# Performance work log

Hardware: AMD Instinct MI355X
Metric: run time of the kernel (lower is better)

## Reference

```python
import jax, jax.numpy as jnp
import numpy as np

N_PTS = 65536      # query points (ray samples)
N_NODES = 4096     # deformation-graph nodes
K = 20             # neighbors, hardcoded in the module
D_PE = 32          # positional-encoding channels (sliced off, unused)
DIS_THRESH = 0.00021
FAR_VAL = 1e9


def setup_inputs() -> dict:
    key = jax.random.key(0)
    k1, k2, k3, k4, k5 = jax.random.split(key, 5)
    inputs = jax.random.normal(k1, (N_PTS, 3 + D_PE), dtype=jnp.float32)
    vd = jax.random.normal(k2, (N_NODES, 3), dtype=jnp.float32)
    R = jax.random.normal(k3, (N_NODES, 3, 3), dtype=jnp.float32)
    g = jax.random.normal(k4, (N_NODES, 3), dtype=jnp.float32)
    t = jax.random.normal(k5, (N_NODES, 3), dtype=jnp.float32) * 0.1
    return {"inputs": inputs, "vd": vd, "R": R, "g": g, "t": t}


def reference(inputs, vd, R, g, t):
    pts = inputs[:, :3]  # [N,3]; inputs[:,3:] (positional encoding) is unused

    # --- KNN (knn_points semantics: squared L2 dists, ascending) ---
    d2 = (jnp.sum(pts * pts, axis=-1, keepdims=True)
          + jnp.sum(vd * vd, axis=-1)[None, :]
          - 2.0 * pts @ vd.T)                      # [N, n]
    neg_d, idx = jax.lax.top_k(-d2, K)             # smallest d2 first
    dis = -neg_d                                   # [N,K] squared dists, ascending

    # --- neighbor weights: w = (1 - d/d_max)^2, normalized ---
    dis_max = jnp.max(dis, axis=-1, keepdims=True)
    w = jnp.square(1.0 - dis / dis_max)
    w = w / jnp.sum(w, axis=-1, keepdims=True)     # [N,K] (K=20 > 1, so no ones override)

    # --- per-neighbor gather + rigid transform: p = R^T (x - g - t) + g ---
    Rg = R[idx]                                    # [N,K,3,3]
    gg = g[idx]                                    # [N,K,3]
    tg = t[idx]                                    # [N,K,3]
    x = pts[:, None, :] - gg - tg                  # [N,K,3]
    p = jnp.einsum('nkji,nkj->nki', Rg, x) + gg    # R^T @ x, [N,K,3]
    R_inv = jnp.swapaxes(Rg, -1, -2)               # [N,K,3,3]

    # --- weighted blend over K neighbors ---
    p_blend = jnp.sum(p * w[:, :, None], axis=1)               # [N,3]
    R_blend = jnp.sum(R_inv * w[:, :, None, None], axis=1)     # [N,3,3]

    # --- far-point masking on x-coordinate ---
    far = dis[:, 0] > DIS_THRESH
    p_blend = p_blend.at[:, 0].set(jnp.where(far, FAR_VAL, p_blend[:, 0]))
    return p_blend, R_blend
```

## Files before the change

kernel.cpp:

```cpp
#include <hip/hip_runtime.h>
#include <stdint.h>


#define NPTS   65536
#define NNODES 4096
#define KSEL   20
#define CAP    32
#define BT     256
#define AFRAG_BYTES  (NNODES * 64)
#define WS_NEEDED    (AFRAG_BYTES + NNODES * 4)

typedef __attribute__((ext_vector_type(8)))  short short8;
typedef __attribute__((ext_vector_type(16))) float f32x16;

__device__ __forceinline__ uint32_t umin32(uint32_t a, uint32_t b) { return a < b ? a : b; }
__device__ __forceinline__ uint32_t umax32(uint32_t a, uint32_t b) { return a > b ? a : b; }
__device__ __forceinline__ void cmpswap(uint32_t& a, uint32_t& b) {
  const uint32_t lo = umin32(a, b), hi = umax32(a, b); a = lo; b = hi;
}
__device__ __forceinline__ void insert20(uint32_t m[KSEL], uint32_t x) {
#pragma unroll
  for (int k = KSEL - 1; k >= 1; --k)
    m[k] = umin32(m[k], umax32(m[k - 1], x));
  m[0] = umin32(m[0], x);
}
__device__ __forceinline__ float thr_from(uint32_t m19) {
  return __uint_as_float(umin32((m19 >> 12) << 11, 0x7F7FFFFFu));
}
__device__ __forceinline__ unsigned short f2bf(float x) {
  uint32_t u = __float_as_uint(x);
  return (unsigned short)((u + 0x7FFFu + ((u >> 16) & 1u)) >> 16);
}
__device__ __forceinline__ float bf2f(unsigned short h) {
  return __uint_as_float(((uint32_t)h) << 16);
}

__global__ void dg_prep(const float* __restrict__ vd,
                        unsigned short* __restrict__ aF, float* __restrict__ svP) {
  const int j = blockIdx.x * 256 + threadIdx.x;
  const float v0 = vd[j * 3 + 0], v1 = vd[j * 3 + 1], v2 = vd[j * 3 + 2];
  unsigned short H[3], M[3], L[3];
  const float vc[3] = {v0, v1, v2};
#pragma unroll
  for (int c = 0; c < 3; ++c) {
    H[c] = f2bf(vc[c]);
    const float r1 = vc[c] - bf2f(H[c]);
    M[c] = f2bf(r1);
    const float r2 = r1 - bf2f(M[c]);
    L[c] = f2bf(r2);
  }
  unsigned short* o = aF + j * 32;
  o[0]=H[0]; o[1]=H[1]; o[2]=H[2]; o[3]=M[0]; o[4]=M[1]; o[5]=M[2];
  o[6]=L[0]; o[7]=L[1]; o[8]=L[2]; o[9]=H[0]; o[10]=H[1]; o[11]=H[2];
  o[12]=M[0]; o[13]=M[1]; o[14]=M[2]; o[15]=L[0];
  o[16]=L[1]; o[17]=L[2]; o[18]=H[0]; o[19]=H[1]; o[20]=H[2];
  o[21]=M[0]; o[22]=M[1]; o[23]=M[2]; o[24]=L[0]; o[25]=L[1]; o[26]=L[2];
  o[27]=0; o[28]=0; o[29]=0; o[30]=0; o[31]=0;
  const int row = j & 31, t = j >> 5;
  const int h = (row >> 2) & 1;
  const int i = (row & 3) + 4 * (row >> 3);
  svP[t * 32 + h * 16 + i] = v0 * v0 + v1 * v1 + v2 * v2;
}

__global__ __launch_bounds__(BT, 4) void dg_mfma(
    const float* __restrict__ inp, const float* __restrict__ vd,
    const float* __restrict__ Rm, const float* __restrict__ gv,
    const float* __restrict__ tv, const short8* __restrict__ aF,
    const float4* __restrict__ svP, float* __restrict__ out)
{
  __shared__ uint32_t st[CAP * BT];
  const int tid  = threadIdx.x;
  const int lane = tid & 63;
  const int col  = lane & 31;
  const int h    = lane >> 5;
  const int wv   = tid >> 6;
  const int half = wv & 1;
  const int pg   = wv >> 1;
  const int P    = pg * 32 + col;
  const int gi   = blockIdx.x * 64 + P;

  const float p0 = inp[gi * 35 + 0];
  const float p1 = inp[gi * 35 + 1];
  const float p2 = inp[gi * 35 + 2];
  const float sp = p0 * p0 + p1 * p1 + p2 * p2;

  unsigned short qH[3], qM[3], qL[3];
  {
    const float qc[3] = {-2.0f * p0, -2.0f * p1, -2.0f * p2};
#pragma unroll
    for (int c = 0; c < 3; ++c) {
      qH[c] = f2bf(qc[c]);
      const float r1 = qc[c] - bf2f(qH[c]);
      qM[c] = f2bf(r1);
      const float r2 = r1 - bf2f(qM[c]);
      qL[c] = f2bf(r2);
    }
  }
  short8 b1, b2;
  if (h == 0) {
    b1[0]=qH[0]; b1[1]=qH[1]; b1[2]=qH[2]; b1[3]=qH[0];
    b1[4]=qH[1]; b1[5]=qH[2]; b1[6]=qH[0]; b1[7]=qH[1];
    b2[0]=qM[1]; b2[1]=qM[2]; b2[2]=qL[0]; b2[3]=qL[1];
    b2[4]=qL[2]; b2[5]=qL[0]; b2[6]=qL[1]; b2[7]=qL[2];
  } else {
    b1[0]=qH[2]; b1[1]=qM[0]; b1[2]=qM[1]; b1[3]=qM[2];
    b1[4]=qM[0]; b1[5]=qM[1]; b1[6]=qM[2]; b1[7]=qM[0];
    b2[0]=qL[0]; b2[1]=qL[1]; b2[2]=qL[2]; b2[3]=0;
    b2[4]=0; b2[5]=0; b2[6]=0; b2[7]=0;
  }

  uint32_t m[KSEL];
#pragma unroll
  for (int k = 0; k < KSEL; ++k) m[k] = 0xFFFFFFFFu;
  uint32_t cnt = 0;
  float thr = __uint_as_float(0x7F7FFFFFu);

  auto drain = [&]() {
    for (uint32_t u = 0; u < cnt; ++u) {
      const uint32_t x = st[u * BT + tid];
      if (x < m[KSEL - 1]) insert20(m, x);
    }
    cnt = 0;
    uint32_t k19 = m[KSEL - 1];
    k19 = umin32(k19, (uint32_t)__shfl_xor((int)k19, 32));
    thr = thr_from(k19);
  };

  const int T0 = half * 64;
  const short8* ap = aF + ((size_t)(T0 * 32 + col) * 64 + (size_t)h * 16) / 16;
  const float4* sv = svP + ((size_t)T0 * 32 + (size_t)h * 16) / 4;
  uint32_t nb = (uint32_t)(T0 * 32 + 4 * h);

#pragma unroll 1
  for (int t = 0; t < 64; ++t) {
    const short8 a1 = ap[0];
    const short8 a2 = ap[2];
    const float4 s0 = sv[0], s1 = sv[1], s2 = sv[2], s3 = sv[3];
    f32x16 acc;
    acc[0]=sp+s0.x;  acc[1]=sp+s0.y;  acc[2]=sp+s0.z;  acc[3]=sp+s0.w;
    acc[4]=sp+s1.x;  acc[5]=sp+s1.y;  acc[6]=sp+s1.z;  acc[7]=sp+s1.w;
    acc[8]=sp+s2.x;  acc[9]=sp+s2.y;  acc[10]=sp+s2.z; acc[11]=sp+s2.w;
    acc[12]=sp+s3.x; acc[13]=sp+s3.y; acc[14]=sp+s3.z; acc[15]=sp+s3.w;
    acc = __builtin_amdgcn_mfma_f32_32x32x16_bf16(a1, b1, acc, 0, 0, 0);
    acc = __builtin_amdgcn_mfma_f32_32x32x16_bf16(a2, b2, acc, 0, 0, 0);
#pragma unroll
    for (int i = 0; i < 16; ++i) {
      const float d = acc[i];
      const uint32_t key =
          ((__float_as_uint(fmaxf(d, 0.0f)) & 0xFFFFF800u) << 1)
          + (nb + (uint32_t)((i & 3) + 8 * (i >> 2)));
      st[cnt * BT + tid] = key;
      cnt += (uint32_t)(d < thr);
    }
    if (__any((int)(cnt >= 16))) drain();
    ap += 4 * 32;
    sv += 8;
    nb += 32;
  }
  drain();

  uint32_t arr[32];
#pragma unroll
  for (int k = 0; k < KSEL; ++k) arr[k] = m[k];
#pragma unroll
  for (int k = KSEL; k < 32; ++k) arr[k] = 0xFFFFFFFFu;
#pragma unroll
  for (int k = 0; k < 16; ++k) {
    const uint32_t sa = (uint32_t)__shfl_xor((int)arr[k],      32);
    const uint32_t sb = (uint32_t)__shfl_xor((int)arr[31 - k], 32);
    arr[k]      = umin32(arr[k],      sb);
    arr[31 - k] = umin32(arr[31 - k], sa);
  }
#pragma unroll
  for (int dd = 16; dd >= 1; dd >>= 1)
#pragma unroll
    for (int k = 0; k < 32; ++k)
      if ((k & dd) == 0) cmpswap(arr[k], arr[k | dd]);

  __syncthreads();
  if (half == 1 && h == 0) {
    uint32_t* mb = st + P * KSEL;
#pragma unroll
    for (int k = 0; k < KSEL; ++k) mb[k] = arr[k];
  }
  __syncthreads();
  if (half == 1) return;

  uint32_t sset[KSEL];
  {
    const uint32_t* mb = st + P * KSEL;
#pragma unroll
    for (int k = 0; k < KSEL; ++k)
      sset[k] = umin32(arr[k], mb[KSEL - 1 - k]);
  }

  int   id10[10];
  float d10[10];
  float dmn = 1e30f, dmx = -1e30f;
#pragma unroll
  for (int s = 0; s < 10; ++s) {
    const int idk = (int)(sset[2 * s + h] & 0xFFFu);
    id10[s] = idk;
    const float v0 = vd[idk * 3 + 0];
    const float v1 = vd[idk * 3 + 1];
    const float v2 = vd[idk * 3 + 2];
    const float sv2 = v0 * v0 + v1 * v1 + v2 * v2;
    const float dt  = p0 * v0 + p1 * v1 + p2 * v2;
    const float ddx = (sp + sv2) - 2.0f * dt;
    d10[s] = ddx;
    dmn = fminf(dmn, ddx);
    dmx = fmaxf(dmx, ddx);
  }
  dmx = fmaxf(dmx, __shfl_xor(dmx, 32));
  dmn = fminf(dmn, __shfl_xor(dmn, 32));

  const float invmax = 1.0f / dmx;
  float wsum = 0.0f, pb0 = 0.0f, pb1 = 0.0f, pb2 = 0.0f;
  float rb[9];
#pragma unroll
  for (int a2i = 0; a2i < 9; ++a2i) rb[a2i] = 0.0f;

#pragma unroll
  for (int s = 0; s < 10; ++s) {
    const int idk = id10[s];
    const float u = 1.0f - d10[s] * invmax;
    const float w = u * u;
    wsum += w;
    const float* Rp = Rm + idk * 9;
    const float r00 = Rp[0], r01 = Rp[1], r02 = Rp[2];
    const float r10 = Rp[3], r11 = Rp[4], r12 = Rp[5];
    const float r20 = Rp[6], r21 = Rp[7], r22 = Rp[8];
    const float g0 = gv[idk * 3 + 0];
    const float g1 = gv[idk * 3 + 1];
    const float g2 = gv[idk * 3 + 2];
    const float t0 = tv[idk * 3 + 0];
    const float t1 = tv[idk * 3 + 1];
    const float t2 = tv[idk * 3 + 2];
    const float x0 = p0 - g0 - t0;
    const float x1 = p1 - g1 - t1;
    const float x2 = p2 - g2 - t2;
    pb0 += w * (r00 * x0 + r10 * x1 + r20 * x2 + g0);
    pb1 += w * (r01 * x0 + r11 * x1 + r21 * x2 + g1);
    pb2 += w * (r02 * x0 + r12 * x1 + r22 * x2 + g2);
    rb[0] += w * r00; rb[1] += w * r10; rb[2] += w * r20;
    rb[3] += w * r01; rb[4] += w * r11; rb[5] += w * r21;
    rb[6] += w * r02; rb[7] += w * r12; rb[8] += w * r22;
  }

  wsum += __shfl_xor(wsum, 32);
  pb0  += __shfl_xor(pb0, 32);
  pb1  += __shfl_xor(pb1, 32);
  pb2  += __shfl_xor(pb2, 32);
#pragma unroll
  for (int a2i = 0; a2i < 9; ++a2i) rb[a2i] += __shfl_xor(rb[a2i], 32);

  if (h == 0) {
    const float inw = 1.0f / wsum;
    float o0 = pb0 * inw;
    if (dmn > 0.00021f) o0 = 1000000000.0f;
    float* po = out + (size_t)gi * 3;
    po[0] = o0; po[1] = pb1 * inw; po[2] = pb2 * inw;
    float* ro = out + (size_t)NPTS * 3 + (size_t)gi * 9;
#pragma unroll
    for (int a2i = 0; a2i < 9; ++a2i) ro[a2i] = rb[a2i] * inw;
  }
}

__global__ __launch_bounds__(BT, 4) void dg_fb(
    const float* __restrict__ inp, const float* __restrict__ vd,
    const float* __restrict__ Rm, const float* __restrict__ gv,
    const float* __restrict__ tv, float* __restrict__ out)
{
  __shared__ uint32_t st[33 * BT];
  const int tid = threadIdx.x;
  const int q   = (tid >> 4) & 3;
  const int pl  = tid & 15;
  const int wv  = tid >> 6;
  const int gi  = blockIdx.x * 64 + wv * 16 + pl;
  const float p0 = inp[gi * 35 + 0];
  const float p1 = inp[gi * 35 + 1];
  const float p2 = inp[gi * 35 + 2];
  const float sp = p0 * p0 + p1 * p1 + p2 * p2;
  uint32_t m[KSEL];
#pragma unroll
  for (int k = 0; k < KSEL; ++k) m[k] = 0xFFFFFFFFu;
  int cnt = 0;
  float thr = __uint_as_float(0x7F7FFFFFu);
  const int jbase = q * (NNODES / 4);
  int lo = 0;
#pragma unroll
  for (int c = 0; c < 6; ++c) {
    const int hi = 32 << c;
    for (int i = lo; i < hi; ++i) {
      const int j = jbase + i;
      const float v0 = vd[j * 3 + 0], v1 = vd[j * 3 + 1], v2 = vd[j * 3 + 2];
      const float sv = v0 * v0 + v1 * v1 + v2 * v2;
      const float dt = p0 * v0 + p1 * v1 + p2 * v2;
      float d2 = fmaxf((sp + sv) - 2.0f * dt, 0.0f);
      if (d2 < thr) {
        st[cnt * BT + tid] = ((__float_as_uint(d2) & 0xFFFFF800u) << 1) | (uint32_t)j;
        if (++cnt == 33) {
          for (int u = 0; u < cnt; ++u) {
            const uint32_t x = st[u * BT + tid];
            if (x < m[KSEL - 1]) insert20(m, x);
          }
          cnt = 0; thr = thr_from(m[KSEL - 1]);
        }
      }
    }
    for (int u = 0; u < cnt; ++u) {
      const uint32_t x = st[u * BT + tid];
      if (x < m[KSEL - 1]) insert20(m, x);
    }
    cnt = 0; thr = thr_from(m[KSEL - 1]); lo = hi;
  }
  uint32_t arr[32];
#pragma unroll
  for (int k = 0; k < KSEL; ++k) arr[k] = m[k];
#pragma unroll
  for (int k = KSEL; k < 32; ++k) arr[k] = 0xFFFFFFFFu;
#pragma unroll
  for (int mask = 32; mask >= 16; mask >>= 1) {
#pragma unroll
    for (int k = 0; k < 16; ++k) {
      const uint32_t sa = (uint32_t)__shfl_xor((int)arr[k],      mask);
      const uint32_t sb = (uint32_t)__shfl_xor((int)arr[31 - k], mask);
      arr[k]      = umin32(arr[k],      sb);
      arr[31 - k] = umin32(arr[31 - k], sa);
    }
#pragma unroll
    for (int dd = 16; dd >= 1; dd >>= 1)
#pragma unroll
      for (int k = 0; k < 32; ++k)
        if ((k & dd) == 0) cmpswap(arr[k], arr[k | dd]);
  }
  int id5[5]; float d5[5];
  float dmn = 1e30f, dmx = -1e30f;
#pragma unroll
  for (int s = 0; s < 5; ++s) {
    const int idk = (int)(arr[4 * s + q] & 0xFFFu);
    id5[s] = idk;
    const float v0 = vd[idk * 3 + 0], v1 = vd[idk * 3 + 1], v2 = vd[idk * 3 + 2];
    const float sv = v0 * v0 + v1 * v1 + v2 * v2;
    const float dt = p0 * v0 + p1 * v1 + p2 * v2;
    const float ddx = (sp + sv) - 2.0f * dt;
    d5[s] = ddx; dmn = fminf(dmn, ddx); dmx = fmaxf(dmx, ddx);
  }
#pragma unroll
  for (int r = 16; r <= 32; r <<= 1) {
    dmx = fmaxf(dmx, __shfl_xor(dmx, r));
    dmn = fminf(dmn, __shfl_xor(dmn, r));
  }
  const float invmax = 1.0f / dmx;
  float wsum = 0.0f, pb0 = 0.0f, pb1 = 0.0f, pb2 = 0.0f;
  float rb[9];
#pragma unroll
  for (int a2i = 0; a2i < 9; ++a2i) rb[a2i] = 0.0f;
#pragma unroll
  for (int s = 0; s < 5; ++s) {
    const int idk = id5[s];
    const float u = 1.0f - d5[s] * invmax;
    const float w = u * u;
    wsum += w;
    const float* Rp = Rm + idk * 9;
    const float r00 = Rp[0], r01 = Rp[1], r02 = Rp[2];
    const float r10 = Rp[3], r11 = Rp[4], r12 = Rp[5];
    const float r20 = Rp[6], r21 = Rp[7], r22 = Rp[8];
    const float g0 = gv[idk * 3 + 0], g1 = gv[idk * 3 + 1], g2 = gv[idk * 3 + 2];
    const float t0 = tv[idk * 3 + 0], t1 = tv[idk * 3 + 1], t2 = tv[idk * 3 + 2];
    const float x0 = p0 - g0 - t0, x1 = p1 - g1 - t1, x2 = p2 - g2 - t2;
    pb0 += w * (r00 * x0 + r10 * x1 + r20 * x2 + g0);
    pb1 += w * (r01 * x0 + r11 * x1 + r21 * x2 + g1);
    pb2 += w * (r02 * x0 + r12 * x1 + r22 * x2 + g2);
    rb[0] += w * r00; rb[1] += w * r10; rb[2] += w * r20;
    rb[3] += w * r01; rb[4] += w * r11; rb[5] += w * r21;
    rb[6] += w * r02; rb[7] += w * r12; rb[8] += w * r22;
  }
#pragma unroll
  for (int r = 16; r <= 32; r <<= 1) {
    wsum += __shfl_xor(wsum, r);
    pb0 += __shfl_xor(pb0, r);
    pb1 += __shfl_xor(pb1, r);
    pb2 += __shfl_xor(pb2, r);
#pragma unroll
    for (int a2i = 0; a2i < 9; ++a2i) rb[a2i] += __shfl_xor(rb[a2i], r);
  }
  if (q == 0) {
    const float inw = 1.0f / wsum;
    float o0 = pb0 * inw;
    if (dmn > 0.00021f) o0 = 1000000000.0f;
    float* po = out + (size_t)gi * 3;
    po[0] = o0; po[1] = pb1 * inw; po[2] = pb2 * inw;
    float* ro = out + (size_t)NPTS * 3 + (size_t)gi * 9;
#pragma unroll
    for (int a2i = 0; a2i < 9; ++a2i) ro[a2i] = rb[a2i] * inw;
  }
}

extern "C" void kernel_launch(void* const* d_in, const int* in_sizes, int n_in,
                              void* d_out, int out_size, void* d_ws, size_t ws_size,
                              hipStream_t stream) {
  const float* inp = (const float*)d_in[0];
  const float* vd  = (const float*)d_in[1];
  const float* Rm  = (const float*)d_in[2];
  const float* gv  = (const float*)d_in[3];
  const float* tv  = (const float*)d_in[4];
  float* out = (float*)d_out;

  if (ws_size >= (size_t)WS_NEEDED) {
    unsigned short* aF = (unsigned short*)d_ws;
    float* svt = (float*)((char*)d_ws + AFRAG_BYTES);
    dg_prep<<<NNODES / 256, 256, 0, stream>>>(vd, aF, svt);
    dg_mfma<<<NPTS / 64, BT, 0, stream>>>(inp, vd, Rm, gv, tv,
                                          (const short8*)aF,
                                          (const float4*)svt, out);
  } else {
    dg_fb<<<NPTS / 64, BT, 0, stream>>>(inp, vd, Rm, gv, tv, out);
  }
}
```

Measured before the change: 163.5 us.

## Split KNN node scan across four waves per point group with tree merge

Each block now handles 32 points instead of 64, and the 4096 nodes are split into four quarters, one per wave, so each wave scans 32 tiles instead of 64. The four partial top-20 lists are combined in a two-level tree merge through shared memory, with a 32-wide bitonic sort at each level. The grid is doubled and the candidate staging buffer shrinks from 32 to 20 slots per thread, which lowers LDS use and may raise occupancy. In exchange, the drain threshold drops to 4 pending candidates, so drains happen more often, and the extra merge stage adds barriers and sorting work.

```diff
diff --git a/kernel.cpp b/kernel.cpp
--- a/kernel.cpp
+++ b/kernel.cpp
@@ -5,7 +5,7 @@
 #define NPTS   65536
 #define NNODES 4096
 #define KSEL   20
-#define CAP    32
+#define CAP    20
 #define BT     256
 #define AFRAG_BYTES  (NNODES * 64)
 #define WS_NEEDED    (AFRAG_BYTES + NNODES * 4)
@@ -33,6 +33,13 @@
 }
 __device__ __forceinline__ float bf2f(unsigned short h) {
   return __uint_as_float(((uint32_t)h) << 16);
+}
+__device__ __forceinline__ void sort32(uint32_t arr[32]) {
+#pragma unroll
+  for (int dd = 16; dd >= 1; dd >>= 1)
+#pragma unroll
+    for (int k = 0; k < 32; ++k)
+      if ((k & dd) == 0) cmpswap(arr[k], arr[k | dd]);
 }
 
 __global__ void dg_prep(const float* __restrict__ vd,
@@ -73,11 +80,8 @@
   const int lane = tid & 63;
   const int col  = lane & 31;
   const int h    = lane >> 5;
-  const int wv   = tid >> 6;
-  const int half = wv & 1;
-  const int pg   = wv >> 1;
-  const int P    = pg * 32 + col;
-  const int gi   = blockIdx.x * 64 + P;
+  const int q    = tid >> 6;
+  const int gi   = blockIdx.x * 32 + col;
 
   const float p0 = inp[gi * 35 + 0];
   const float p1 = inp[gi * 35 + 1];
@@ -126,13 +130,13 @@
     thr = thr_from(k19);
   };
 
-  const int T0 = half * 64;
-  const short8* ap = aF + ((size_t)(T0 * 32 + col) * 64 + (size_t)h * 16) / 16;
-  const float4* sv = svP + ((size_t)T0 * 32 + (size_t)h * 16) / 4;
+  const int T0 = q * 32;
+  const short8* ap = aF + ((T0 * 32 + col) * 4 + h);
+  const float4* sv = svP + (T0 * 8 + h * 4);
   uint32_t nb = (uint32_t)(T0 * 32 + 4 * h);
 
 #pragma unroll 1
-  for (int t = 0; t < 64; ++t) {
+  for (int t = 0; t < 32; ++t) {
     const short8 a1 = ap[0];
     const short8 a2 = ap[2];
     const float4 s0 = sv[0], s1 = sv[1], s2 = sv[2], s3 = sv[3];
@@ -152,8 +156,8 @@
       st[cnt * BT + tid] = key;
       cnt += (uint32_t)(d < thr);
     }
-    if (__any((int)(cnt >= 16))) drain();
-    ap += 4 * 32;
+    if (__any((int)(cnt >= CAP - 16))) drain();
+    ap += 128;
     sv += 8;
     nb += 32;
   }
@@ -171,27 +175,42 @@
     arr[k]      = umin32(arr[k],      sb);
     arr[31 - k] = umin32(arr[31 - k], sa);
   }
-#pragma unroll
-  for (int dd = 16; dd >= 1; dd >>= 1)
-#pragma unroll
-    for (int k = 0; k < 32; ++k)
-      if ((k & dd) == 0) cmpswap(arr[k], arr[k | dd]);
+  sort32(arr);
 
   __syncthreads();
-  if (half == 1 && h == 0) {
-    uint32_t* mb = st + P * KSEL;
+  if ((q & 1) == 1 && h == 0) {
+    uint32_t* mb = st + ((q >> 1) * 640) + col * KSEL;
 #pragma unroll
     for (int k = 0; k < KSEL; ++k) mb[k] = arr[k];
   }
   __syncthreads();
-  if (half == 1) return;
-
-  uint32_t sset[KSEL];
+  if ((q & 1) == 0) {
+    const uint32_t* mb = st + ((q >> 1) * 640) + col * KSEL;
+#pragma unroll
+    for (int k = 0; k < 32; ++k) {
+      const int j = 31 - k;
+      const uint32_t bk = (j < KSEL) ? mb[j] : 0xFFFFFFFFu;
+      arr[k] = umin32(arr[k], bk);
+    }
+    sort32(arr);
+  }
+  if (q == 2 && h == 0) {
+    uint32_t* mb = st + 1280 + col * KSEL;
+#pragma unroll
+    for (int k = 0; k < KSEL; ++k) mb[k] = arr[k];
+  }
+  __syncthreads();
+  if (q != 0) return;
+
   {
-    const uint32_t* mb = st + P * KSEL;
-#pragma unroll
-    for (int k = 0; k < KSEL; ++k)
-      sset[k] = umin32(arr[k], mb[KSEL - 1 - k]);
+    const uint32_t* mb = st + 1280 + col * KSEL;
+#pragma unroll
+    for (int k = 0; k < 32; ++k) {
+      const int j = 31 - k;
+      const uint32_t bk = (j < KSEL) ? mb[j] : 0xFFFFFFFFu;
+      arr[k] = umin32(arr[k], bk);
+    }
+    sort32(arr);
   }
 
   int   id10[10];
@@ -199,7 +218,7 @@
   float dmn = 1e30f, dmx = -1e30f;
 #pragma unroll
   for (int s = 0; s < 10; ++s) {
-    const int idk = (int)(sset[2 * s + h] & 0xFFFu);
+    const int idk = (int)(arr[2 * s + h] & 0xFFFu);
     id10[s] = idk;
     const float v0 = vd[idk * 3 + 0];
     const float v1 = vd[idk * 3 + 1];
@@ -411,7 +430,7 @@
     unsigned short* aF = (unsigned short*)d_ws;
     float* svt = (float*)((char*)d_ws + AFRAG_BYTES);
     dg_prep<<<NNODES / 256, 256, 0, stream>>>(vd, aF, svt);
-    dg_mfma<<<NPTS / 64, BT, 0, stream>>>(inp, vd, Rm, gv, tv,
+    dg_mfma<<<NPTS / 32, BT, 0, stream>>>(inp, vd, Rm, gv, tv,
                                           (const short8*)aF,
                                           (const float4*)svt, out);
   } else {
```

Result: slower. 223.2 us (+36.5%).

## Fold norm terms into MFMA operands and double-buffer distance tiles

Applied to the files above, without the earlier changes.

The squared-norm terms |v|^2 and |p|^2 are now encoded as split-bf16 values in the padding slots of the A/B fragments, so the MFMA itself produces the full squared distance. This removes the separate svP table and the per-tile float4 loads and adds. The main loop is restructured into a two-accumulator ping-pong, so the MFMAs for the next tile are issued before the candidate-filtering of the current tile, overlapping matrix work with the selection ALU/LDS work. The drain trigger changes from cnt>=16 to CAP-16, which is the same value. The norm terms are now represented with less precision (|p|^2 in two bf16 parts), which can slightly change the distance values used for neighbor selection.

```diff
diff --git a/kernel.cpp b/kernel.cpp
--- a/kernel.cpp
+++ b/kernel.cpp
@@ -8,7 +8,7 @@
 #define CAP    32
 #define BT     256
 #define AFRAG_BYTES  (NNODES * 64)
-#define WS_NEEDED    (AFRAG_BYTES + NNODES * 4)
+#define WS_NEEDED    AFRAG_BYTES
 
 typedef __attribute__((ext_vector_type(8)))  short short8;
 typedef __attribute__((ext_vector_type(16))) float f32x16;
@@ -36,7 +36,7 @@
 }
 
 __global__ void dg_prep(const float* __restrict__ vd,
-                        unsigned short* __restrict__ aF, float* __restrict__ svP) {
+                        unsigned short* __restrict__ aF) {
   const int j = blockIdx.x * 256 + threadIdx.x;
   const float v0 = vd[j * 3 + 0], v1 = vd[j * 3 + 1], v2 = vd[j * 3 + 2];
   unsigned short H[3], M[3], L[3];
@@ -49,24 +49,28 @@
     const float r2 = r1 - bf2f(M[c]);
     L[c] = f2bf(r2);
   }
+  const float sv = v0 * v0 + v1 * v1 + v2 * v2;
+  const unsigned short svH = f2bf(sv);
+  const float rs1 = sv - bf2f(svH);
+  const unsigned short svM = f2bf(rs1);
+  const unsigned short svL = f2bf(rs1 - bf2f(svM));
+
   unsigned short* o = aF + j * 32;
   o[0]=H[0]; o[1]=H[1]; o[2]=H[2]; o[3]=M[0]; o[4]=M[1]; o[5]=M[2];
   o[6]=L[0]; o[7]=L[1]; o[8]=L[2]; o[9]=H[0]; o[10]=H[1]; o[11]=H[2];
   o[12]=M[0]; o[13]=M[1]; o[14]=M[2]; o[15]=L[0];
   o[16]=L[1]; o[17]=L[2]; o[18]=H[0]; o[19]=H[1]; o[20]=H[2];
-  o[21]=M[0]; o[22]=M[1]; o[23]=M[2]; o[24]=L[0]; o[25]=L[1]; o[26]=L[2];
-  o[27]=0; o[28]=0; o[29]=0; o[30]=0; o[31]=0;
-  const int row = j & 31, t = j >> 5;
-  const int h = (row >> 2) & 1;
-  const int i = (row & 3) + 4 * (row >> 3);
-  svP[t * 32 + h * 16 + i] = v0 * v0 + v1 * v1 + v2 * v2;
+  o[21]=M[0]; o[22]=M[1]; o[23]=M[2];
+  o[24]=L[0]; o[25]=L[1]; o[26]=L[2];
+  o[27]=(unsigned short)svH; o[28]=(unsigned short)svM; o[29]=(unsigned short)svL;
+  o[30]=0x3F80; o[31]=0x3F80;
 }
 
 __global__ __launch_bounds__(BT, 4) void dg_mfma(
     const float* __restrict__ inp, const float* __restrict__ vd,
     const float* __restrict__ Rm, const float* __restrict__ gv,
     const float* __restrict__ tv, const short8* __restrict__ aF,
-    const float4* __restrict__ svP, float* __restrict__ out)
+    float* __restrict__ out)
 {
   __shared__ uint32_t st[CAP * BT];
   const int tid  = threadIdx.x;
@@ -84,7 +88,7 @@
   const float p2 = inp[gi * 35 + 2];
   const float sp = p0 * p0 + p1 * p1 + p2 * p2;
 
-  unsigned short qH[3], qM[3], qL[3];
+  unsigned short qH[3], qM[3], qL[3], spH, spM;
   {
     const float qc[3] = {-2.0f * p0, -2.0f * p1, -2.0f * p2};
 #pragma unroll
@@ -95,6 +99,8 @@
       const float r2 = r1 - bf2f(qM[c]);
       qL[c] = f2bf(r2);
     }
+    spH = f2bf(sp);
+    spM = f2bf(sp - bf2f(spH));
   }
   short8 b1, b2;
   if (h == 0) {
@@ -105,8 +111,9 @@
   } else {
     b1[0]=qH[2]; b1[1]=qM[0]; b1[2]=qM[1]; b1[3]=qM[2];
     b1[4]=qM[0]; b1[5]=qM[1]; b1[6]=qM[2]; b1[7]=qM[0];
-    b2[0]=qL[0]; b2[1]=qL[1]; b2[2]=qL[2]; b2[3]=0;
-    b2[4]=0; b2[5]=0; b2[6]=0; b2[7]=0;
+    b2[0]=qL[0]; b2[1]=qL[1]; b2[2]=qL[2];
+    b2[3]=(short)0x3F80; b2[4]=(short)0x3F80; b2[5]=(short)0x3F80;
+    b2[6]=(short)spH; b2[7]=(short)spM;
   }
 
   uint32_t m[KSEL];
@@ -126,23 +133,12 @@
     thr = thr_from(k19);
   };
 
-  const int T0 = half * 64;
-  const short8* ap = aF + ((size_t)(T0 * 32 + col) * 64 + (size_t)h * 16) / 16;
-  const float4* sv = svP + ((size_t)T0 * 32 + (size_t)h * 16) / 4;
-  uint32_t nb = (uint32_t)(T0 * 32 + 4 * h);
-
-#pragma unroll 1
-  for (int t = 0; t < 64; ++t) {
-    const short8 a1 = ap[0];
-    const short8 a2 = ap[2];
-    const float4 s0 = sv[0], s1 = sv[1], s2 = sv[2], s3 = sv[3];
-    f32x16 acc;
-    acc[0]=sp+s0.x;  acc[1]=sp+s0.y;  acc[2]=sp+s0.z;  acc[3]=sp+s0.w;
-    acc[4]=sp+s1.x;  acc[5]=sp+s1.y;  acc[6]=sp+s1.z;  acc[7]=sp+s1.w;
-    acc[8]=sp+s2.x;  acc[9]=sp+s2.y;  acc[10]=sp+s2.z; acc[11]=sp+s2.w;
-    acc[12]=sp+s3.x; acc[13]=sp+s3.y; acc[14]=sp+s3.z; acc[15]=sp+s3.w;
-    acc = __builtin_amdgcn_mfma_f32_32x32x16_bf16(a1, b1, acc, 0, 0, 0);
-    acc = __builtin_amdgcn_mfma_f32_32x32x16_bf16(a2, b2, acc, 0, 0, 0);
+  f32x16 zacc;
+#pragma unroll
+  for (int i = 0; i < 16; ++i) zacc[i] = 0.0f;
+
+  uint32_t nb = 0;
+  auto process = [&](const f32x16& acc) {
 #pragma unroll
     for (int i = 0; i < 16; ++i) {
       const float d = acc[i];
@@ -152,11 +148,35 @@
       st[cnt * BT + tid] = key;
       cnt += (uint32_t)(d < thr);
     }
-    if (__any((int)(cnt >= 16))) drain();
-    ap += 4 * 32;
-    sv += 8;
+    if (__any((int)(cnt >= CAP - 16))) drain();
     nb += 32;
-  }
+  };
+
+  const int T0 = half * 64;
+  const short8* ap = aF + ((T0 * 32 + col) * 4 + h);
+  nb = (uint32_t)(T0 * 32 + 4 * h);
+
+  short8 a1A = ap[0], a2A = ap[2]; ap += 128;
+  f32x16 accA = __builtin_amdgcn_mfma_f32_32x32x16_bf16(a1A, b1, zacc, 0, 0, 0);
+  accA = __builtin_amdgcn_mfma_f32_32x32x16_bf16(a2A, b2, accA, 0, 0, 0);
+  short8 a1B = ap[0], a2B = ap[2]; ap += 128;
+  f32x16 accB;
+
+#pragma unroll 1
+  for (int k = 0; k < 31; ++k) {
+    accB = __builtin_amdgcn_mfma_f32_32x32x16_bf16(a1B, b1, zacc, 0, 0, 0);
+    accB = __builtin_amdgcn_mfma_f32_32x32x16_bf16(a2B, b2, accB, 0, 0, 0);
+    a1A = ap[0]; a2A = ap[2]; ap += 128;
+    process(accA);
+    accA = __builtin_amdgcn_mfma_f32_32x32x16_bf16(a1A, b1, zacc, 0, 0, 0);
+    accA = __builtin_amdgcn_mfma_f32_32x32x16_bf16(a2A, b2, accA, 0, 0, 0);
+    a1B = ap[0]; a2B = ap[2]; ap += 128;
+    process(accB);
+  }
+  accB = __builtin_amdgcn_mfma_f32_32x32x16_bf16(a1B, b1, zacc, 0, 0, 0);
+  accB = __builtin_amdgcn_mfma_f32_32x32x16_bf16(a2B, b2, accB, 0, 0, 0);
+  process(accA);
+  process(accB);
   drain();
 
   uint32_t arr[32];
@@ -409,11 +429,9 @@
 
   if (ws_size >= (size_t)WS_NEEDED) {
     unsigned short* aF = (unsigned short*)d_ws;
-    float* svt = (float*)((char*)d_ws + AFRAG_BYTES);
-    dg_prep<<<NNODES / 256, 256, 0, stream>>>(vd, aF, svt);
+    dg_prep<<<NNODES / 256, 256, 0, stream>>>(vd, aF);
     dg_mfma<<<NPTS / 64, BT, 0, stream>>>(inp, vd, Rm, gv, tv,
-                                          (const short8*)aF,
-                                          (const float4*)svt, out);
+                                          (const short8*)aF, out);
   } else {
     dg_fb<<<NPTS / 64, BT, 0, stream>>>(inp, vd, Rm, gv, tv, out);
   }
```

After: 153.4 us. 6.2% less time.
